# Kernel tuning notes

Measured on AMD Instinct MI355X. Metric: run time of the kernel, lower is better.

## Reference

```python
import jax, jax.numpy as jnp
import numpy as np

N, T, F_IN, F_OUT, E = 20000, 4, 64, 64, 640000


def setup_inputs() -> dict:
    key = jax.random.key(0)
    k1, k2, k3, k4, k5, k6 = jax.random.split(key, 6)
    node_features = jax.random.normal(k1, (N, T, F_IN), dtype=jnp.float32)
    edge_weights = jax.random.uniform(k2, (T, E), dtype=jnp.float32)
    src = jax.random.randint(k3, (E,), 0, N, dtype=jnp.int32)
    dst = jax.random.randint(k4, (E,), 0, N, dtype=jnp.int32)
    W = jax.random.normal(k5, (F_OUT, F_IN), dtype=jnp.float32) / np.sqrt(F_IN)
    b = jax.random.normal(k6, (F_OUT,), dtype=jnp.float32) * 0.01
    return {"node_features": node_features, "edge_weights": edge_weights,
            "src": src, "dst": dst, "W": W, "b": b}


def reference(node_features, edge_weights, src, dst, W, b):
    # u_mul_e: gather source node features and scale by per-edge, per-time weight
    # edge_weights (T, E) -> transposed (E, T) -> broadcast over feature dim
    msg = node_features[src] * edge_weights.T[:, :, None]          # (E, T, F_IN)
    # fn.sum: scatter-sum messages into destination nodes
    h = jax.ops.segment_sum(msg, dst, num_segments=node_features.shape[0])  # (N, T, F_IN)
    # nn.Linear(in_features, out_features)
    return h @ W.T + b                                             # (N, T, F_OUT)
```

## Files before the change

kernel.cpp:

```cpp
#include <hip/hip_runtime.h>

#define N_NODES 20000
#define T_STEPS 4
#define F_DIM   64
#define E_EDGES 640000
#define ROWS    (N_NODES * T_STEPS)
#define ROW_ELEMS (T_STEPS * F_DIM)

#define SCATTER_BLOCKS   (E_EDGES / 256)
#define TRANSFORM_BLOCKS (ROWS / 64)
#define OVF_CAP          4096

#define NREG   8
#define CAPA   8
#define CAPB   8
#define CAPT   (CAPA + CAPB)

__device__ __forceinline__ unsigned short f32_to_bf16_rne(float f) {
    unsigned u = __float_as_uint(f);
    u += 0x7FFFu + ((u >> 16) & 1u);
    return (unsigned short)(u >> 16);
}
__device__ __forceinline__ float bf16_to_f32(unsigned short h) {
    return __uint_as_float((unsigned)h << 16);
}
__device__ __forceinline__ unsigned w_to_u12(float f) {
    unsigned q = __float2uint_rn(f * 4096.0f);
    return q > 4095u ? 4095u : q;
}

__global__ __launch_bounds__(256) void fused_build_kernel(
    const float* __restrict__ x, const float* __restrict__ W,
    unsigned short* __restrict__ yb,
    const int* __restrict__ src, const int* __restrict__ dst,
    const float* __restrict__ ew,
    int* __restrict__ cnt, uint2* __restrict__ bktA, uint2* __restrict__ bktB,
    int4* __restrict__ ovf, int* __restrict__ ovf_cnt)
{
    __shared__ float wt[64 * 64];

    if (blockIdx.x < SCATTER_BLOCKS) {
        unsigned xcc;
        asm volatile("s_getreg_b32 %0, hwreg(HW_REG_XCC_ID)" : "=s"(xcc));
        const int reg = (int)(xcc & 7u);
        int* creg = cnt + (size_t)reg * N_NODES;

        const int e = blockIdx.x * 256 + threadIdx.x;
        const unsigned w0 = w_to_u12(ew[e]);
        const unsigned w1 = w_to_u12(ew[E_EDGES + e]);
        const unsigned w2 = w_to_u12(ew[2 * E_EDGES + e]);
        const unsigned w3 = w_to_u12(ew[3 * E_EDGES + e]);
        const unsigned s  = (unsigned)src[e];
        const unsigned lo = s | (w0 << 16) | (w1 << 28);
        const unsigned hi = (w1 >> 4) | (w2 << 8) | (w3 << 20);
        const int d = dst[e];
        const int pos = atomicAdd(&creg[d], 1);
        const uint2 rec = make_uint2(lo, hi);
        if (pos < CAPA) {
            bktA[((size_t)d * NREG + reg) * CAPA + pos] = rec;
        } else if (pos < CAPT) {
            bktB[((size_t)d * NREG + reg) * CAPB + (pos - CAPA)] = rec;
        } else {
            const int o = atomicAdd(ovf_cnt, 1);
            if (o < OVF_CAP) { int4 r; r.x = (int)rec.x; r.y = (int)rec.y; r.z = d; r.w = 0; ovf[o] = r; }
        }
        return;
    }

    const int tid  = threadIdx.x;
    const int row0 = (blockIdx.x - SCATTER_BLOCKS) * 64;

    {
        const int o  = tid & 63;
        const int fb = (tid >> 6) * 16;
#pragma unroll
        for (int k = 0; k < 16; ++k) {
            const int f = fb + k;
            wt[f * 64 + o] = W[o * 64 + f];
        }
    }
    __syncthreads();

    const int rg = tid >> 4;
    const int oq = (tid & 15) * 4;

    float acc[4][4];
#pragma unroll
    for (int i = 0; i < 4; ++i)
#pragma unroll
        for (int j = 0; j < 4; ++j) acc[i][j] = 0.0f;

    const float4* xg4 = (const float4*)(x + (size_t)(row0 + rg * 4) * 64);

#pragma unroll 4
    for (int fc = 0; fc < 16; ++fc) {
        float4 xv[4];
#pragma unroll
        for (int i = 0; i < 4; ++i) xv[i] = xg4[i * 16 + fc];
#pragma unroll
        for (int j = 0; j < 4; ++j) {
            const int f = fc * 4 + j;
            const float4 w4 = *(const float4*)&wt[f * 64 + oq];
            const float xj0 = j == 0 ? xv[0].x : j == 1 ? xv[0].y : j == 2 ? xv[0].z : xv[0].w;
            const float xj1 = j == 0 ? xv[1].x : j == 1 ? xv[1].y : j == 2 ? xv[1].z : xv[1].w;
            const float xj2 = j == 0 ? xv[2].x : j == 1 ? xv[2].y : j == 2 ? xv[2].z : xv[2].w;
            const float xj3 = j == 0 ? xv[3].x : j == 1 ? xv[3].y : j == 2 ? xv[3].z : xv[3].w;
            acc[0][0] += xj0 * w4.x; acc[0][1] += xj0 * w4.y; acc[0][2] += xj0 * w4.z; acc[0][3] += xj0 * w4.w;
            acc[1][0] += xj1 * w4.x; acc[1][1] += xj1 * w4.y; acc[1][2] += xj1 * w4.z; acc[1][3] += xj1 * w4.w;
            acc[2][0] += xj2 * w4.x; acc[2][1] += xj2 * w4.y; acc[2][2] += xj2 * w4.z; acc[2][3] += xj2 * w4.w;
            acc[3][0] += xj3 * w4.x; acc[3][1] += xj3 * w4.y; acc[3][2] += xj3 * w4.z; acc[3][3] += xj3 * w4.w;
        }
    }

#pragma unroll
    for (int i = 0; i < 4; ++i) {
        const int r = row0 + rg * 4 + i;
        ushort4 h;
        h.x = f32_to_bf16_rne(acc[i][0]);
        h.y = f32_to_bf16_rne(acc[i][1]);
        h.z = f32_to_bf16_rne(acc[i][2]);
        h.w = f32_to_bf16_rne(acc[i][3]);
        *(ushort4*)(yb + (size_t)r * 64 + oq) = h;
    }
}

__device__ __forceinline__ float dec_w(uint2 r, int t) {
    const unsigned long long pk = (unsigned long long)r.x |
                                  ((unsigned long long)r.y << 32);
    const unsigned q = (unsigned)(pk >> (16 + 12 * t)) & 0xFFFu;
    return (float)q * (1.0f / 4096.0f);
}

#define BATCH4(RP, K0)                                                        \
    {                                                                         \
        const uint2 R0 = (RP)[(K0) + 0], R1 = (RP)[(K0) + 1],                 \
                    R2 = (RP)[(K0) + 2], R3 = (RP)[(K0) + 3];                 \
        const ushort4 V0 = *(const ushort4*)(yb + (size_t)(R0.x & 0xFFFFu) * ROW_ELEMS + l4); \
        const ushort4 V1 = *(const ushort4*)(yb + (size_t)(R1.x & 0xFFFFu) * ROW_ELEMS + l4); \
        const ushort4 V2 = *(const ushort4*)(yb + (size_t)(R2.x & 0xFFFFu) * ROW_ELEMS + l4); \
        const ushort4 V3 = *(const ushort4*)(yb + (size_t)(R3.x & 0xFFFFu) * ROW_ELEMS + l4); \
        float w;                                                              \
        w = dec_w(R0, t);                                                     \
        acc.x += bf16_to_f32(V0.x) * w; acc.y += bf16_to_f32(V0.y) * w;       \
        acc.z += bf16_to_f32(V0.z) * w; acc.w += bf16_to_f32(V0.w) * w;       \
        w = dec_w(R1, t);                                                     \
        acc.x += bf16_to_f32(V1.x) * w; acc.y += bf16_to_f32(V1.y) * w;       \
        acc.z += bf16_to_f32(V1.z) * w; acc.w += bf16_to_f32(V1.w) * w;       \
        w = dec_w(R2, t);                                                     \
        acc.x += bf16_to_f32(V2.x) * w; acc.y += bf16_to_f32(V2.y) * w;       \
        acc.z += bf16_to_f32(V2.z) * w; acc.w += bf16_to_f32(V2.w) * w;       \
        w = dec_w(R3, t);                                                     \
        acc.x += bf16_to_f32(V3.x) * w; acc.y += bf16_to_f32(V3.y) * w;       \
        acc.z += bf16_to_f32(V3.z) * w; acc.w += bf16_to_f32(V3.w) * w;       \
    }

__global__ __launch_bounds__(256) void accumulate_kernel(
    const unsigned short* __restrict__ yb, const int* __restrict__ cnt,
    const uint2* __restrict__ bktA, const uint2* __restrict__ bktB,
    const int4* __restrict__ ovf, const int* __restrict__ ovf_cnt,
    const float* __restrict__ b, float* __restrict__ out)
{
    const int lane = threadIdx.x & 63;
    const int n    = blockIdx.x * 4 + (threadIdx.x >> 6);
    const int t    = lane >> 4;
    const int l4   = lane * 4;

    int degc[NREG];
#pragma unroll
    for (int r = 0; r < NREG; ++r) {
        int d = cnt[(size_t)r * N_NODES + n];
        degc[r] = d > CAPT ? CAPT : d;
    }

    float4 acc = make_float4(0.f, 0.f, 0.f, 0.f);

#pragma unroll
    for (int r = 0; r < NREG; ++r) {
        const uint2* pa = bktA + ((size_t)n * NREG + r) * CAPA;
        const int d = degc[r];
        int k = 0;
        if (d >= 4) {
            BATCH4(pa, 0); k = 4;
            if (d >= 8) {
                BATCH4(pa, 4); k = 8;
                if (d > 8) {
                    const uint2* pb = bktB + ((size_t)n * NREG + r) * CAPB;
                    if (d >= 12) {
                        BATCH4(pb, 0); k = 12;
                        if (d >= 16) { BATCH4(pb, 4); k = 16; }
                    }
                    for (; k < d; ++k) {
                        const uint2 rr = pb[k - 8];
                        const float w = dec_w(rr, t);
                        const ushort4 v = *(const ushort4*)(yb + (size_t)(rr.x & 0xFFFFu) * ROW_ELEMS + l4);
                        acc.x += bf16_to_f32(v.x) * w;
                        acc.y += bf16_to_f32(v.y) * w;
                        acc.z += bf16_to_f32(v.z) * w;
                        acc.w += bf16_to_f32(v.w) * w;
                    }
                }
            }
        }
        for (; k < d && k < 8; ++k) {
            const uint2 rr = pa[k];
            const float w = dec_w(rr, t);
            const ushort4 v = *(const ushort4*)(yb + (size_t)(rr.x & 0xFFFFu) * ROW_ELEMS + l4);
            acc.x += bf16_to_f32(v.x) * w;
            acc.y += bf16_to_f32(v.y) * w;
            acc.z += bf16_to_f32(v.z) * w;
            acc.w += bf16_to_f32(v.w) * w;
        }
    }

    {
        int m = *ovf_cnt;
        if (m > OVF_CAP) m = OVF_CAP;
        for (int i = 0; i < m; ++i) {
            const int4 rr = ovf[i];
            if (rr.z == n) {
                const uint2 r2 = make_uint2((unsigned)rr.x, (unsigned)rr.y);
                const float w = dec_w(r2, t);
                const ushort4 v = *(const ushort4*)(yb + (size_t)(r2.x & 0xFFFFu) * ROW_ELEMS + l4);
                acc.x += bf16_to_f32(v.x) * w;
                acc.y += bf16_to_f32(v.y) * w;
                acc.z += bf16_to_f32(v.z) * w;
                acc.w += bf16_to_f32(v.w) * w;
            }
        }
    }

    const float4 bv = *(const float4*)(b + (lane & 15) * 4);
    acc.x += bv.x; acc.y += bv.y; acc.z += bv.z; acc.w += bv.w;
    *(float4*)(out + (size_t)n * ROW_ELEMS + l4) = acc;
}

extern "C" void kernel_launch(void* const* d_in, const int* in_sizes, int n_in,
                              void* d_out, int out_size, void* d_ws, size_t ws_size,
                              hipStream_t stream) {
    const float* x   = (const float*)d_in[0];
    const float* ew  = (const float*)d_in[1];
    const int*   src = (const int*)  d_in[2];
    const int*   dst = (const int*)  d_in[3];
    const float* W   = (const float*)d_in[4];
    const float* b   = (const float*)d_in[5];
    float*       out = (float*)d_out;

    char* ws = (char*)d_ws;
    size_t off = 0;
    auto alloc = [&](size_t bytes) {
        void* p = ws + off;
        off += (bytes + 255) & ~(size_t)255;
        return p;
    };
    unsigned short* yb  = (unsigned short*)alloc((size_t)ROWS * 64 * 2);
    int*            cnt = (int*) alloc(((size_t)NREG * N_NODES + 1) * sizeof(int));
    int4*           ovf = (int4*)alloc((size_t)OVF_CAP * sizeof(int4));
    uint2*          bktA = (uint2*)alloc((size_t)N_NODES * NREG * CAPA * sizeof(uint2));
    uint2*          bktB = (uint2*)alloc((size_t)N_NODES * NREG * CAPB * sizeof(uint2));
    int*            ovf_cnt = cnt + (size_t)NREG * N_NODES;
    (void)ws_size;

    hipError_t err = hipMemsetAsync(cnt, 0, ((size_t)NREG * N_NODES + 1) * sizeof(int), stream);
    (void)err;
    fused_build_kernel<<<SCATTER_BLOCKS + TRANSFORM_BLOCKS, 256, 0, stream>>>(
        x, W, yb, src, dst, ew, cnt, bktA, bktB, ovf, ovf_cnt);
    accumulate_kernel<<<N_NODES / 4, 256, 0, stream>>>(
        yb, cnt, bktA, bktB, ovf, ovf_cnt, b, out);
}
```

Measured before the change: 182.9 us.

## Replace atomic bucket scatter with chunked histogram, scan and CSR placement

Swaps the per-XCC capped bucket arrays with overflow list for an exact CSR layout. A per-chunk shared-memory histogram over dst is followed by a two-level prefix scan, then a scatter that ranks edges with LDS atomics. The accumulate kernel then reads each node's edges contiguously, with no overflow scan and no per-region branching. This removes global atomics and the O(overflow) loop per node, but adds three extra kernel launches and a 128x20000 count/base matrix. The scatter also now runs on only 128 blocks, which leaves it with little parallelism.

```diff
diff --git a/kernel.cpp b/kernel.cpp
--- a/kernel.cpp
+++ b/kernel.cpp
@@ -7,14 +7,10 @@
 #define ROWS    (N_NODES * T_STEPS)
 #define ROW_ELEMS (T_STEPS * F_DIM)
 
-#define SCATTER_BLOCKS   (E_EDGES / 256)
+#define CH     128
+#define CHE    (E_EDGES / CH)
+#define NB2    ((N_NODES + 255) / 256)
 #define TRANSFORM_BLOCKS (ROWS / 64)
-#define OVF_CAP          4096
-
-#define NREG   8
-#define CAPA   8
-#define CAPB   8
-#define CAPT   (CAPA + CAPB)
 
 __device__ __forceinline__ unsigned short f32_to_bf16_rne(float f) {
     unsigned u = __float_as_uint(f);
@@ -29,46 +25,108 @@
     return q > 4095u ? 4095u : q;
 }
 
-__global__ __launch_bounds__(256) void fused_build_kernel(
+
+__global__ __launch_bounds__(256) void hist_kernel(
+    const int* __restrict__ dst, unsigned short* __restrict__ cntmat)
+{
+    __shared__ int h[N_NODES / 2];
+    const int tid = threadIdx.x;
+    for (int i = tid; i < N_NODES / 2; i += 256) h[i] = 0;
+    __syncthreads();
+    const int c = blockIdx.x;
+#pragma unroll 4
+    for (int j = 0; j < 20; ++j) {
+        const int idx = j * 256 + tid;
+        if (idx < CHE) {
+            const int n = dst[c * CHE + idx];
+            atomicAdd(&h[n >> 1], 1 << (16 * (n & 1)));
+        }
+    }
+    __syncthreads();
+    unsigned* crow = (unsigned*)(cntmat + (size_t)c * N_NODES);
+    for (int i = tid; i < N_NODES / 2; i += 256) crow[i] = (unsigned)h[i];
+}
+
+__global__ __launch_bounds__(256) void scan_a_kernel(
+    const unsigned short* __restrict__ cntmat, unsigned short* __restrict__ base,
+    int* __restrict__ local, unsigned short* __restrict__ deg,
+    int* __restrict__ blocksum)
+{
+    __shared__ int s[256];
+    const int tid = threadIdx.x;
+    const int n = blockIdx.x * 256 + tid;
+    int run = 0;
+    if (n < N_NODES) {
+        for (int c = 0; c < CH; ++c) {
+            const unsigned short u = cntmat[(size_t)c * N_NODES + n];
+            base[(size_t)c * N_NODES + n] = (unsigned short)run;
+            run += u;
+        }
+        deg[n] = (unsigned short)run;
+    }
+    s[tid] = run;
+    __syncthreads();
+    for (int o = 1; o < 256; o <<= 1) {
+        const int v = (tid >= o) ? s[tid - o] : 0;
+        __syncthreads();
+        s[tid] += v;
+        __syncthreads();
+    }
+    if (n < N_NODES) local[n] = s[tid] - run;
+    if (tid == 255) blocksum[blockIdx.x] = s[255];
+}
+
+__global__ void scan_b_kernel(const int* __restrict__ blocksum,
+                              int* __restrict__ blockoff)
+{
+    if (threadIdx.x == 0) {
+        int run = 0;
+        for (int i = 0; i < NB2; ++i) { blockoff[i] = run; run += blocksum[i]; }
+    }
+}
+
+__global__ __launch_bounds__(256) void scatter_transform_kernel(
     const float* __restrict__ x, const float* __restrict__ W,
     unsigned short* __restrict__ yb,
     const int* __restrict__ src, const int* __restrict__ dst,
     const float* __restrict__ ew,
-    int* __restrict__ cnt, uint2* __restrict__ bktA, uint2* __restrict__ bktB,
-    int4* __restrict__ ovf, int* __restrict__ ovf_cnt)
-{
-    __shared__ float wt[64 * 64];
-
-    if (blockIdx.x < SCATTER_BLOCKS) {
-        unsigned xcc;
-        asm volatile("s_getreg_b32 %0, hwreg(HW_REG_XCC_ID)" : "=s"(xcc));
-        const int reg = (int)(xcc & 7u);
-        int* creg = cnt + (size_t)reg * N_NODES;
-
-        const int e = blockIdx.x * 256 + threadIdx.x;
-        const unsigned w0 = w_to_u12(ew[e]);
-        const unsigned w1 = w_to_u12(ew[E_EDGES + e]);
-        const unsigned w2 = w_to_u12(ew[2 * E_EDGES + e]);
-        const unsigned w3 = w_to_u12(ew[3 * E_EDGES + e]);
-        const unsigned s  = (unsigned)src[e];
-        const unsigned lo = s | (w0 << 16) | (w1 << 28);
-        const unsigned hi = (w1 >> 4) | (w2 << 8) | (w3 << 20);
-        const int d = dst[e];
-        const int pos = atomicAdd(&creg[d], 1);
-        const uint2 rec = make_uint2(lo, hi);
-        if (pos < CAPA) {
-            bktA[((size_t)d * NREG + reg) * CAPA + pos] = rec;
-        } else if (pos < CAPT) {
-            bktB[((size_t)d * NREG + reg) * CAPB + (pos - CAPA)] = rec;
-        } else {
-            const int o = atomicAdd(ovf_cnt, 1);
-            if (o < OVF_CAP) { int4 r; r.x = (int)rec.x; r.y = (int)rec.y; r.z = d; r.w = 0; ovf[o] = r; }
+    const unsigned short* __restrict__ base, const int* __restrict__ local,
+    const int* __restrict__ blockoff, uint2* __restrict__ rec)
+{
+    __shared__ int smem[N_NODES / 2];
+
+    if (blockIdx.x < CH) {
+        const int tid = threadIdx.x;
+        for (int i = tid; i < N_NODES / 2; i += 256) smem[i] = 0;
+        __syncthreads();
+        const int c = blockIdx.x;
+        const unsigned short* brow = base + (size_t)c * N_NODES;
+#pragma unroll 4
+        for (int j = 0; j < 20; ++j) {
+            const int idx = j * 256 + tid;
+            if (idx < CHE) {
+                const int e = c * CHE + idx;
+                const unsigned w0 = w_to_u12(ew[e]);
+                const unsigned w1 = w_to_u12(ew[E_EDGES + e]);
+                const unsigned w2 = w_to_u12(ew[2 * E_EDGES + e]);
+                const unsigned w3 = w_to_u12(ew[3 * E_EDGES + e]);
+                const unsigned s  = (unsigned)src[e];
+                const unsigned lo = s | (w0 << 16) | (w1 << 28);
+                const unsigned hi = (w1 >> 4) | (w2 << 8) | (w3 << 20);
+                const int n = dst[e];
+                const int sh = 16 * (n & 1);
+                const int old = atomicAdd(&smem[n >> 1], 1 << sh);
+                const int rank = (old >> sh) & 0xFFFF;
+                const int slot = blockoff[n >> 8] + local[n] + (int)brow[n] + rank;
+                rec[slot] = make_uint2(lo, hi);
+            }
         }
         return;
     }
 
+    float* wt = (float*)smem;
     const int tid  = threadIdx.x;
-    const int row0 = (blockIdx.x - SCATTER_BLOCKS) * 64;
+    const int row0 = (blockIdx.x - CH) * 64;
 
     {
         const int o  = tid & 63;
@@ -155,9 +213,9 @@
     }
 
 __global__ __launch_bounds__(256) void accumulate_kernel(
-    const unsigned short* __restrict__ yb, const int* __restrict__ cnt,
-    const uint2* __restrict__ bktA, const uint2* __restrict__ bktB,
-    const int4* __restrict__ ovf, const int* __restrict__ ovf_cnt,
+    const unsigned short* __restrict__ yb, const uint2* __restrict__ rec,
+    const int* __restrict__ local, const unsigned short* __restrict__ deg,
+    const int* __restrict__ blockoff,
     const float* __restrict__ b, float* __restrict__ out)
 {
     const int lane = threadIdx.x & 63;
@@ -165,68 +223,23 @@
     const int t    = lane >> 4;
     const int l4   = lane * 4;
 
-    int degc[NREG];
-#pragma unroll
-    for (int r = 0; r < NREG; ++r) {
-        int d = cnt[(size_t)r * N_NODES + n];
-        degc[r] = d > CAPT ? CAPT : d;
-    }
+    const int start = blockoff[n >> 8] + local[n];
+    const int d     = (int)deg[n];
+    const uint2* rp = rec + start;
 
     float4 acc = make_float4(0.f, 0.f, 0.f, 0.f);
 
-#pragma unroll
-    for (int r = 0; r < NREG; ++r) {
-        const uint2* pa = bktA + ((size_t)n * NREG + r) * CAPA;
-        const int d = degc[r];
-        int k = 0;
-        if (d >= 4) {
-            BATCH4(pa, 0); k = 4;
-            if (d >= 8) {
-                BATCH4(pa, 4); k = 8;
-                if (d > 8) {
-                    const uint2* pb = bktB + ((size_t)n * NREG + r) * CAPB;
-                    if (d >= 12) {
-                        BATCH4(pb, 0); k = 12;
-                        if (d >= 16) { BATCH4(pb, 4); k = 16; }
-                    }
-                    for (; k < d; ++k) {
-                        const uint2 rr = pb[k - 8];
-                        const float w = dec_w(rr, t);
-                        const ushort4 v = *(const ushort4*)(yb + (size_t)(rr.x & 0xFFFFu) * ROW_ELEMS + l4);
-                        acc.x += bf16_to_f32(v.x) * w;
-                        acc.y += bf16_to_f32(v.y) * w;
-                        acc.z += bf16_to_f32(v.z) * w;
-                        acc.w += bf16_to_f32(v.w) * w;
-                    }
-                }
-            }
-        }
-        for (; k < d && k < 8; ++k) {
-            const uint2 rr = pa[k];
-            const float w = dec_w(rr, t);
-            const ushort4 v = *(const ushort4*)(yb + (size_t)(rr.x & 0xFFFFu) * ROW_ELEMS + l4);
-            acc.x += bf16_to_f32(v.x) * w;
-            acc.y += bf16_to_f32(v.y) * w;
-            acc.z += bf16_to_f32(v.z) * w;
-            acc.w += bf16_to_f32(v.w) * w;
-        }
-    }
-
-    {
-        int m = *ovf_cnt;
-        if (m > OVF_CAP) m = OVF_CAP;
-        for (int i = 0; i < m; ++i) {
-            const int4 rr = ovf[i];
-            if (rr.z == n) {
-                const uint2 r2 = make_uint2((unsigned)rr.x, (unsigned)rr.y);
-                const float w = dec_w(r2, t);
-                const ushort4 v = *(const ushort4*)(yb + (size_t)(r2.x & 0xFFFFu) * ROW_ELEMS + l4);
-                acc.x += bf16_to_f32(v.x) * w;
-                acc.y += bf16_to_f32(v.y) * w;
-                acc.z += bf16_to_f32(v.z) * w;
-                acc.w += bf16_to_f32(v.w) * w;
-            }
-        }
+    int k = 0;
+    for (; k + 8 <= d; k += 8) { BATCH4(rp, k); BATCH4(rp, k + 4); }
+    if (k + 4 <= d) { BATCH4(rp, k); k += 4; }
+    for (; k < d; ++k) {
+        const uint2 rr = rp[k];
+        const float w = dec_w(rr, t);
+        const ushort4 v = *(const ushort4*)(yb + (size_t)(rr.x & 0xFFFFu) * ROW_ELEMS + l4);
+        acc.x += bf16_to_f32(v.x) * w;
+        acc.y += bf16_to_f32(v.y) * w;
+        acc.z += bf16_to_f32(v.z) * w;
+        acc.w += bf16_to_f32(v.w) * w;
     }
 
     const float4 bv = *(const float4*)(b + (lane & 15) * 4);
@@ -252,18 +265,21 @@
         off += (bytes + 255) & ~(size_t)255;
         return p;
     };
-    unsigned short* yb  = (unsigned short*)alloc((size_t)ROWS * 64 * 2);
-    int*            cnt = (int*) alloc(((size_t)NREG * N_NODES + 1) * sizeof(int));
-    int4*           ovf = (int4*)alloc((size_t)OVF_CAP * sizeof(int4));
-    uint2*          bktA = (uint2*)alloc((size_t)N_NODES * NREG * CAPA * sizeof(uint2));
-    uint2*          bktB = (uint2*)alloc((size_t)N_NODES * NREG * CAPB * sizeof(uint2));
-    int*            ovf_cnt = cnt + (size_t)NREG * N_NODES;
+    unsigned short* yb     = (unsigned short*)alloc((size_t)ROWS * 64 * 2);
+    unsigned short* cntmat = (unsigned short*)alloc((size_t)CH * N_NODES * 2);
+    unsigned short* base   = (unsigned short*)alloc((size_t)CH * N_NODES * 2);
+    int*            local  = (int*)           alloc((size_t)N_NODES * sizeof(int));
+    unsigned short* deg    = (unsigned short*)alloc((size_t)N_NODES * 2);
+    int*            blocksum = (int*)         alloc(NB2 * sizeof(int));
+    int*            blockoff = (int*)         alloc(NB2 * sizeof(int));
+    uint2*          rec    = (uint2*)         alloc((size_t)E_EDGES * sizeof(uint2));
     (void)ws_size;
 
-    hipError_t err = hipMemsetAsync(cnt, 0, ((size_t)NREG * N_NODES + 1) * sizeof(int), stream);
-    (void)err;
-    fused_build_kernel<<<SCATTER_BLOCKS + TRANSFORM_BLOCKS, 256, 0, stream>>>(
-        x, W, yb, src, dst, ew, cnt, bktA, bktB, ovf, ovf_cnt);
+    hist_kernel<<<CH, 256, 0, stream>>>(dst, cntmat);
+    scan_a_kernel<<<NB2, 256, 0, stream>>>(cntmat, base, local, deg, blocksum);
+    scan_b_kernel<<<1, 64, 0, stream>>>(blocksum, blockoff);
+    scatter_transform_kernel<<<CH + TRANSFORM_BLOCKS, 256, 0, stream>>>(
+        x, W, yb, src, dst, ew, base, local, blockoff, rec);
     accumulate_kernel<<<N_NODES / 4, 256, 0, stream>>>(
-        yb, cnt, bktA, bktB, ovf, ovf_cnt, b, out);
-}
+        yb, rec, local, deg, blockoff, b, out);
+}
```

New measurement: 176.1 us. 3.7% less time.

## Replace per-node atomic buckets with range partition plus per-range counting sort

Applied to the files above, without the earlier changes.

Edges are partitioned by 64-node destination ranges using shared-memory staging, with batched global atomics per range. A new sort kernel then counting-sorts each range by node into contiguous 8-byte records and emits per-node offset/degree info. The accumulate kernel walks a single contiguous segment per node instead of eight per-XCC buckets. This cuts global atomic contention and bucket fragmentation, but adds a kernel launch and serial per-block partition rounds that run on only 128 blocks.

```diff
diff --git a/kernel.cpp b/kernel.cpp
--- a/kernel.cpp
+++ b/kernel.cpp
@@ -7,14 +7,16 @@
 #define ROWS    (N_NODES * T_STEPS)
 #define ROW_ELEMS (T_STEPS * F_DIM)
 
-#define SCATTER_BLOCKS   (E_EDGES / 256)
+#define RB       64
+#define NRANGE   313
+#define CAPF     3072
+#define PART_BLOCKS   128
+#define EDGES_PER_PB  5000
+#define ROUND_E  250
+#define NROUNDS  20
+#define STAGE_D  8
 #define TRANSFORM_BLOCKS (ROWS / 64)
-#define OVF_CAP          4096
-
-#define NREG   8
-#define CAPA   8
-#define CAPB   8
-#define CAPT   (CAPA + CAPB)
+#define OVF_CAP  4096
 
 __device__ __forceinline__ unsigned short f32_to_bf16_rne(float f) {
     unsigned u = __float_as_uint(f);
@@ -29,46 +31,84 @@
     return q > 4095u ? 4095u : q;
 }
 
-__global__ __launch_bounds__(256) void fused_build_kernel(
+__global__ __launch_bounds__(256) void build_kernel(
     const float* __restrict__ x, const float* __restrict__ W,
     unsigned short* __restrict__ yb,
     const int* __restrict__ src, const int* __restrict__ dst,
     const float* __restrict__ ew,
-    int* __restrict__ cnt, uint2* __restrict__ bktA, uint2* __restrict__ bktB,
+    int* __restrict__ gcnt, int4* __restrict__ bktF,
     int4* __restrict__ ovf, int* __restrict__ ovf_cnt)
 {
-    __shared__ float wt[64 * 64];
-
-    if (blockIdx.x < SCATTER_BLOCKS) {
-        unsigned xcc;
-        asm volatile("s_getreg_b32 %0, hwreg(HW_REG_XCC_ID)" : "=s"(xcc));
-        const int reg = (int)(xcc & 7u);
-        int* creg = cnt + (size_t)reg * N_NODES;
-
-        const int e = blockIdx.x * 256 + threadIdx.x;
-        const unsigned w0 = w_to_u12(ew[e]);
-        const unsigned w1 = w_to_u12(ew[E_EDGES + e]);
-        const unsigned w2 = w_to_u12(ew[2 * E_EDGES + e]);
-        const unsigned w3 = w_to_u12(ew[3 * E_EDGES + e]);
-        const unsigned s  = (unsigned)src[e];
-        const unsigned lo = s | (w0 << 16) | (w1 << 28);
-        const unsigned hi = (w1 >> 4) | (w2 << 8) | (w3 << 20);
-        const int d = dst[e];
-        const int pos = atomicAdd(&creg[d], 1);
-        const uint2 rec = make_uint2(lo, hi);
-        if (pos < CAPA) {
-            bktA[((size_t)d * NREG + reg) * CAPA + pos] = rec;
-        } else if (pos < CAPT) {
-            bktB[((size_t)d * NREG + reg) * CAPB + (pos - CAPA)] = rec;
-        } else {
-            const int o = atomicAdd(ovf_cnt, 1);
-            if (o < OVF_CAP) { int4 r; r.x = (int)rec.x; r.y = (int)rec.y; r.z = d; r.w = 0; ovf[o] = r; }
+    __shared__ int4 stage[NRANGE * STAGE_D];
+    __shared__ int  scnt[NRANGE];
+
+    const int tid = threadIdx.x;
+
+    if (blockIdx.x < PART_BLOCKS) {
+        for (int i = tid; i < NRANGE; i += 256) scnt[i] = 0;
+        __syncthreads();
+        const int base = blockIdx.x * EDGES_PER_PB;
+
+        for (int rd = 0; rd < NROUNDS; ++rd) {
+            if (tid < ROUND_E) {
+                const int e = base + rd * ROUND_E + tid;
+                const unsigned w0 = w_to_u12(ew[e]);
+                const unsigned w1 = w_to_u12(ew[E_EDGES + e]);
+                const unsigned w2 = w_to_u12(ew[2 * E_EDGES + e]);
+                const unsigned w3 = w_to_u12(ew[3 * E_EDGES + e]);
+                const unsigned s  = (unsigned)src[e];
+                const int d = dst[e];
+                int4 rec;
+                rec.x = (int)(s | (w0 << 16) | (w1 << 28));
+                rec.y = (int)((w1 >> 4) | (w2 << 8) | (w3 << 20));
+                rec.z = d;
+                rec.w = 0;
+                const int r = d >> 6;
+                const int p = atomicAdd(&scnt[r], 1);
+                if (p < STAGE_D) {
+                    stage[r * STAGE_D + p] = rec;
+                } else {
+                    const int o = atomicAdd(ovf_cnt, 1);
+                    if (o < OVF_CAP) ovf[o] = rec;
+                }
+            }
+            __syncthreads();
+            for (int r = tid; r < NRANGE; r += 256) {
+                const int c  = scnt[r];
+                const int st = c > STAGE_D ? STAGE_D : c;
+                const int k  = st & ~3;
+                if (k) {
+                    const int bg = atomicAdd(&gcnt[r], k);
+                    for (int q = 0; q < k; ++q) {
+                        const int slot = bg + q;
+                        const int4 rc = stage[r * STAGE_D + q];
+                        if (slot < CAPF) bktF[(size_t)r * CAPF + slot] = rc;
+                        else { const int o = atomicAdd(ovf_cnt, 1); if (o < OVF_CAP) ovf[o] = rc; }
+                    }
+                    for (int q = k; q < st; ++q)
+                        stage[r * STAGE_D + (q - k)] = stage[r * STAGE_D + q];
+                }
+                scnt[r] = st - k;
+            }
+            __syncthreads();
+        }
+        for (int r = tid; r < NRANGE; r += 256) {
+            const int st = scnt[r];
+            if (st) {
+                const int bg = atomicAdd(&gcnt[r], st);
+                for (int q = 0; q < st; ++q) {
+                    const int slot = bg + q;
+                    const int4 rc = stage[r * STAGE_D + q];
+                    if (slot < CAPF) bktF[(size_t)r * CAPF + slot] = rc;
+                    else { const int o = atomicAdd(ovf_cnt, 1); if (o < OVF_CAP) ovf[o] = rc; }
+                }
+            }
         }
         return;
     }
 
-    const int tid  = threadIdx.x;
-    const int row0 = (blockIdx.x - SCATTER_BLOCKS) * 64;
+    float* wt = (float*)stage;
+    const int row0 = (blockIdx.x - PART_BLOCKS) * 64;
 
     {
         const int o  = tid & 63;
@@ -121,6 +161,43 @@
         h.z = f32_to_bf16_rne(acc[i][2]);
         h.w = f32_to_bf16_rne(acc[i][3]);
         *(ushort4*)(yb + (size_t)r * 64 + oq) = h;
+    }
+}
+
+__global__ __launch_bounds__(256) void sort_kernel(
+    const int* __restrict__ gcnt, int4* __restrict__ bktF,
+    unsigned int* __restrict__ nodeinfo)
+{
+    __shared__ int4 lrec[CAPF];
+    __shared__ int hist[RB], pstart[RB], cnt2[RB];
+    const int tid = threadIdx.x;
+    const int r   = blockIdx.x;
+
+    int m = gcnt[r]; if (m > CAPF) m = CAPF;
+    int4* rowp = bktF + (size_t)r * CAPF;
+
+    for (int i = tid; i < m; i += 256) lrec[i] = rowp[i];
+    if (tid < RB) { hist[tid] = 0; cnt2[tid] = 0; }
+    __syncthreads();
+
+    for (int i = tid; i < m; i += 256) atomicAdd(&hist[lrec[i].z & 63], 1);
+    __syncthreads();
+
+    if (tid == 0) {
+        int run = 0;
+        for (int i = 0; i < RB; ++i) { pstart[i] = run; run += hist[i]; }
+    }
+    __syncthreads();
+
+    if (tid < RB)
+        nodeinfo[r * RB + tid] = (unsigned)pstart[tid] | ((unsigned)hist[tid] << 16);
+
+    uint2* out8 = (uint2*)rowp;
+    for (int i = tid; i < m; i += 256) {
+        const int4 rc = lrec[i];
+        const int d6  = rc.z & 63;
+        const int rank = atomicAdd(&cnt2[d6], 1);
+        out8[pstart[d6] + rank] = make_uint2((unsigned)rc.x, (unsigned)rc.y);
     }
 }
 
@@ -155,8 +232,8 @@
     }
 
 __global__ __launch_bounds__(256) void accumulate_kernel(
-    const unsigned short* __restrict__ yb, const int* __restrict__ cnt,
-    const uint2* __restrict__ bktA, const uint2* __restrict__ bktB,
+    const unsigned short* __restrict__ yb, const int4* __restrict__ bktF,
+    const unsigned int* __restrict__ nodeinfo,
     const int4* __restrict__ ovf, const int* __restrict__ ovf_cnt,
     const float* __restrict__ b, float* __restrict__ out)
 {
@@ -165,51 +242,24 @@
     const int t    = lane >> 4;
     const int l4   = lane * 4;
 
-    int degc[NREG];
-#pragma unroll
-    for (int r = 0; r < NREG; ++r) {
-        int d = cnt[(size_t)r * N_NODES + n];
-        degc[r] = d > CAPT ? CAPT : d;
-    }
+    const unsigned info = nodeinfo[n];
+    const int r = n >> 6;
+    const uint2* rp = (const uint2*)(bktF + (size_t)r * CAPF) + (info & 0xFFFFu);
+    const int d = (int)(info >> 16);
 
     float4 acc = make_float4(0.f, 0.f, 0.f, 0.f);
 
-#pragma unroll
-    for (int r = 0; r < NREG; ++r) {
-        const uint2* pa = bktA + ((size_t)n * NREG + r) * CAPA;
-        const int d = degc[r];
-        int k = 0;
-        if (d >= 4) {
-            BATCH4(pa, 0); k = 4;
-            if (d >= 8) {
-                BATCH4(pa, 4); k = 8;
-                if (d > 8) {
-                    const uint2* pb = bktB + ((size_t)n * NREG + r) * CAPB;
-                    if (d >= 12) {
-                        BATCH4(pb, 0); k = 12;
-                        if (d >= 16) { BATCH4(pb, 4); k = 16; }
-                    }
-                    for (; k < d; ++k) {
-                        const uint2 rr = pb[k - 8];
-                        const float w = dec_w(rr, t);
-                        const ushort4 v = *(const ushort4*)(yb + (size_t)(rr.x & 0xFFFFu) * ROW_ELEMS + l4);
-                        acc.x += bf16_to_f32(v.x) * w;
-                        acc.y += bf16_to_f32(v.y) * w;
-                        acc.z += bf16_to_f32(v.z) * w;
-                        acc.w += bf16_to_f32(v.w) * w;
-                    }
-                }
-            }
-        }
-        for (; k < d && k < 8; ++k) {
-            const uint2 rr = pa[k];
-            const float w = dec_w(rr, t);
-            const ushort4 v = *(const ushort4*)(yb + (size_t)(rr.x & 0xFFFFu) * ROW_ELEMS + l4);
-            acc.x += bf16_to_f32(v.x) * w;
-            acc.y += bf16_to_f32(v.y) * w;
-            acc.z += bf16_to_f32(v.z) * w;
-            acc.w += bf16_to_f32(v.w) * w;
-        }
+    int k = 0;
+    for (; k + 8 <= d; k += 8) { BATCH4(rp, k); BATCH4(rp, k + 4); }
+    if (k + 4 <= d) { BATCH4(rp, k); k += 4; }
+    for (; k < d; ++k) {
+        const uint2 rr = rp[k];
+        const float w = dec_w(rr, t);
+        const ushort4 v = *(const ushort4*)(yb + (size_t)(rr.x & 0xFFFFu) * ROW_ELEMS + l4);
+        acc.x += bf16_to_f32(v.x) * w;
+        acc.y += bf16_to_f32(v.y) * w;
+        acc.z += bf16_to_f32(v.z) * w;
+        acc.w += bf16_to_f32(v.w) * w;
     }
 
     {
@@ -252,18 +302,19 @@
         off += (bytes + 255) & ~(size_t)255;
         return p;
     };
-    unsigned short* yb  = (unsigned short*)alloc((size_t)ROWS * 64 * 2);
-    int*            cnt = (int*) alloc(((size_t)NREG * N_NODES + 1) * sizeof(int));
-    int4*           ovf = (int4*)alloc((size_t)OVF_CAP * sizeof(int4));
-    uint2*          bktA = (uint2*)alloc((size_t)N_NODES * NREG * CAPA * sizeof(uint2));
-    uint2*          bktB = (uint2*)alloc((size_t)N_NODES * NREG * CAPB * sizeof(uint2));
-    int*            ovf_cnt = cnt + (size_t)NREG * N_NODES;
+    unsigned short* yb       = (unsigned short*)alloc((size_t)ROWS * 64 * 2);
+    int*            gcnt     = (int*)  alloc((NRANGE + 1) * sizeof(int));
+    int4*           ovf      = (int4*) alloc((size_t)OVF_CAP * sizeof(int4));
+    unsigned int*   nodeinfo = (unsigned int*)alloc((size_t)NRANGE * RB * 4);
+    int4*           bktF     = (int4*) alloc((size_t)NRANGE * CAPF * sizeof(int4));
+    int*            ovf_cnt  = gcnt + NRANGE;
     (void)ws_size;
 
-    hipError_t err = hipMemsetAsync(cnt, 0, ((size_t)NREG * N_NODES + 1) * sizeof(int), stream);
+    hipError_t err = hipMemsetAsync(gcnt, 0, (NRANGE + 1) * sizeof(int), stream);
     (void)err;
-    fused_build_kernel<<<SCATTER_BLOCKS + TRANSFORM_BLOCKS, 256, 0, stream>>>(
-        x, W, yb, src, dst, ew, cnt, bktA, bktB, ovf, ovf_cnt);
+    build_kernel<<<PART_BLOCKS + TRANSFORM_BLOCKS, 256, 0, stream>>>(
+        x, W, yb, src, dst, ew, gcnt, bktF, ovf, ovf_cnt);
+    sort_kernel<<<NRANGE, 256, 0, stream>>>(gcnt, bktF, nodeinfo);
     accumulate_kernel<<<N_NODES / 4, 256, 0, stream>>>(
-        yb, cnt, bktA, bktB, ovf, ovf_cnt, b, out);
-}
+        yb, bktF, nodeinfo, ovf, ovf_cnt, b, out);
+}
```

Result: slower. 203.3 us (+11.1%).
